# Kernel optimization log

Hardware: AMD Instinct MI355X
Metric: run time of the kernel (lower is better)

Reference implementation:

```python
import jax, jax.numpy as jnp
import numpy as np


def setup_inputs() -> dict:
    key = jax.random.key(0)
    k1, k2, k3 = jax.random.split(key, 3)
    b, n, d, f = 16, 2048, 256, 256
    features = jax.random.normal(k1, (b, n, d), dtype=jnp.float32)
    # dense adjacency; row-normalize like MeanAggregator's normalized A
    A = jax.random.uniform(k2, (b, n, n), dtype=jnp.float32)
    A = A / jnp.sum(A, axis=-1, keepdims=True)
    weight = jax.random.normal(k3, (2 * d, f), dtype=jnp.float32) * (1.0 / np.sqrt(2 * d))
    bias = jnp.zeros((f,), dtype=jnp.float32)
    return {"features": features, "A": A, "weight": weight, "bias": bias}


def reference(features, A, weight, bias):
    # agg = A @ features  (MeanAggregator: row-normalized adjacency)
    agg = jnp.einsum('bnm,bmd->bnd', A, features)  # [b,n,d]
    d = features.shape[-1]
    # split-weight GEMM instead of materializing concat:
    # [feat, agg] @ W == feat @ W[:d] + agg @ W[d:]
    out = (jnp.einsum('bnd,df->bnf', features, weight[:d])
           + jnp.einsum('bnd,df->bnf', agg, weight[d:])
           + bias)
    return jax.nn.relu(out)
```

## Files before the change

### kernel.cpp

```cpp
#include <hip/hip_runtime.h>

typedef __attribute__((ext_vector_type(8))) short bf16x8;
typedef __attribute__((ext_vector_type(4))) float f32x4;

__device__ __forceinline__ unsigned short f2bf(float f) {
    unsigned int u = __builtin_bit_cast(unsigned int, f);
    unsigned int r = (u + 0x7FFFu + ((u >> 16) & 1u)) >> 16;
    return (unsigned short)r;
}

__device__ __forceinline__ void gll16(const void* g, void* l) {
    __builtin_amdgcn_global_load_lds(
        (const __attribute__((address_space(1))) void*)g,
        (__attribute__((address_space(3))) void*)l, 16, 0, 0);
}

__global__ __launch_bounds__(256) void transpose_cvt_kernel(
    const float* __restrict__ src, unsigned short* __restrict__ dstT,
    unsigned short* __restrict__ dstS, int R, int C)
{
    __shared__ float tile[64][65];
    const int b = blockIdx.z;
    const float* s = src + (size_t)b * R * C;
    const int r0 = blockIdx.x * 64, c0 = blockIdx.y * 64;
    const int t = threadIdx.x;
    const int r = t >> 2, cg = (t & 3) * 16;

    float v[16];
    const float4* p = reinterpret_cast<const float4*>(s + (size_t)(r0 + r) * C + c0 + cg);
#pragma unroll
    for (int i = 0; i < 4; ++i) {
        float4 q = p[i];
        v[4 * i + 0] = q.x; v[4 * i + 1] = q.y; v[4 * i + 2] = q.z; v[4 * i + 3] = q.w;
    }
#pragma unroll
    for (int i = 0; i < 16; ++i) tile[r][cg + i] = v[i];

    if (dstS) {
        unsigned int w[8];
#pragma unroll
        for (int i = 0; i < 8; ++i)
            w[i] = (unsigned)f2bf(v[2 * i]) | ((unsigned)f2bf(v[2 * i + 1]) << 16);
        unsigned int* d = reinterpret_cast<unsigned int*>(
            dstS + (size_t)b * R * C + (size_t)(r0 + r) * C + c0 + cg);
        *reinterpret_cast<uint4*>(d)     = make_uint4(w[0], w[1], w[2], w[3]);
        *reinterpret_cast<uint4*>(d + 4) = make_uint4(w[4], w[5], w[6], w[7]);
    }

    __syncthreads();

    const int cl = t >> 2, rg = (t & 3) * 16;
    unsigned int w[8];
#pragma unroll
    for (int i = 0; i < 8; ++i) {
        unsigned short lo = f2bf(tile[rg + 2 * i][cl]);
        unsigned short hi = f2bf(tile[rg + 2 * i + 1][cl]);
        w[i] = (unsigned)lo | ((unsigned)hi << 16);
    }
    unsigned int* d = reinterpret_cast<unsigned int*>(
        dstT + (size_t)b * R * C + (size_t)(c0 + cl) * R + r0 + rg);
    *reinterpret_cast<uint4*>(d)     = make_uint4(w[0], w[1], w[2], w[3]);
    *reinterpret_cast<uint4*>(d + 4) = make_uint4(w[4], w[5], w[6], w[7]);
}

__global__ __launch_bounds__(512, 2) void k1_agg_gemm(
    const float* __restrict__ A, const unsigned short* __restrict__ Ft,
    unsigned short* __restrict__ agg)
{
    __shared__ short Ab[2][128][64];
    __shared__ short Bb[2][256][64];

    const int tid = threadIdx.x;
    const int lane = tid & 63, wid = tid >> 6;
    const int wr = wid >> 2, wc = wid & 3;
    const int lo = lane & 15, hi = lane >> 4;
    const int batch = blockIdx.y, mt = blockIdx.x;

    const float* Abase = A + ((size_t)batch * 2048 + (size_t)mt * 128) * 2048;
    const unsigned short* Fbase = Ft + (size_t)batch * 256 * 2048;

    const int arow = tid >> 2;
    const int acg = tid & 3;

    f32x4 acc[4][4];
#pragma unroll
    for (int m = 0; m < 4; ++m)
#pragma unroll
        for (int n = 0; n < 4; ++n) acc[m][n] = (f32x4){0.f, 0.f, 0.f, 0.f};

    float va[16];

    auto load_A = [&](int k0) {
        const float4* p = reinterpret_cast<const float4*>(
            Abase + (size_t)arow * 2048 + k0 + acg * 16);
#pragma unroll
        for (int i = 0; i < 4; ++i) {
            float4 q = p[i];
            va[4 * i + 0] = q.x; va[4 * i + 1] = q.y; va[4 * i + 2] = q.z; va[4 * i + 3] = q.w;
        }
    };
    auto write_A = [&](int buf) {
#pragma unroll
        for (int j = 0; j < 2; ++j) {
            unsigned int w[4];
#pragma unroll
            for (int i = 0; i < 4; ++i) {
                int e = j * 8 + i * 2;
                w[i] = (unsigned)f2bf(va[e]) | ((unsigned)f2bf(va[e + 1]) << 16);
            }
            int slin = acg * 2 + j;
            int off = arow * 64 + ((slin ^ (arow & 7)) << 3);
            *reinterpret_cast<uint4*>(&Ab[buf][0][0] + off) = make_uint4(w[0], w[1], w[2], w[3]);
        }
    };
    auto stage_B = [&](int buf, int k0) {
#pragma unroll
        for (int it = 0; it < 4; ++it) {
            int si = it * 512 + tid;
            int row = si >> 3, slot = si & 7;
            const unsigned short* g = Fbase + (size_t)row * 2048 + k0 + ((slot ^ (row & 7)) << 3);
            short* l = &Bb[buf][0][0] + (size_t)(it * 512 + (wid << 6)) * 8;
            gll16(g, l);
        }
    };

    load_A(0);
    stage_B(0, 0);
    write_A(0);
    __syncthreads();

    for (int t = 0; t < 32; ++t) {
        const int cur = t & 1;
        const int nxt = cur ^ 1;
        const bool has_next = (t + 1) < 32;
        if (has_next) {
            load_A((t + 1) * 64);
            stage_B(nxt, (t + 1) * 64);
        }
#pragma unroll
        for (int kk = 0; kk < 2; ++kk) {
            bf16x8 af[4], bfv[4];
#pragma unroll
            for (int m = 0; m < 4; ++m) {
                int row = wr * 64 + m * 16 + lo;
                int off = row * 64 + (((kk * 4 + hi) ^ (row & 7)) << 3);
                af[m] = *reinterpret_cast<const bf16x8*>(&Ab[cur][0][0] + off);
            }
#pragma unroll
            for (int n = 0; n < 4; ++n) {
                int row = wc * 64 + n * 16 + lo;
                int off = row * 64 + (((kk * 4 + hi) ^ (row & 7)) << 3);
                bfv[n] = *reinterpret_cast<const bf16x8*>(&Bb[cur][0][0] + off);
            }
#pragma unroll
            for (int m = 0; m < 4; ++m)
#pragma unroll
                for (int n = 0; n < 4; ++n)
                    acc[m][n] = __builtin_amdgcn_mfma_f32_16x16x32_bf16(af[m], bfv[n], acc[m][n], 0, 0, 0);
        }
        if (has_next) write_A(nxt);
        __syncthreads();
    }

    unsigned short* obase = agg + ((size_t)batch * 2048 + (size_t)mt * 128) * 256;
#pragma unroll
    for (int m = 0; m < 4; ++m) {
#pragma unroll
        for (int n = 0; n < 4; ++n) {
            int col = wc * 64 + n * 16 + lo;
#pragma unroll
            for (int j = 0; j < 4; ++j) {
                int row = wr * 64 + m * 16 + hi * 4 + j;
                obase[(size_t)row * 256 + col] = f2bf(acc[m][n][j]);
            }
        }
    }
}

__global__ __launch_bounds__(512, 2) void k2_out_gemm(
    const unsigned short* __restrict__ Fb, const unsigned short* __restrict__ aggp,
    const unsigned short* __restrict__ Wt, const float* __restrict__ bias,
    float* __restrict__ out)
{
    __shared__ short Ab[2][128][64];
    __shared__ short Bb[2][256][64];

    const int tid = threadIdx.x;
    const int lane = tid & 63, wid = tid >> 6;
    const int wr = wid >> 2, wc = wid & 3;
    const int lo = lane & 15, hi = lane >> 4;
    const int m0 = blockIdx.x * 128;

    auto stage_A = [&](int buf, int k0) {
        const unsigned short* src = (k0 < 256) ? Fb : aggp;
        const int kk0 = k0 & 255;
#pragma unroll
        for (int it = 0; it < 2; ++it) {
            int si = it * 512 + tid;
            int row = si >> 3, slot = si & 7;
            const unsigned short* g = src + (size_t)(m0 + row) * 256 + kk0 + ((slot ^ (row & 7)) << 3);
            short* l = &Ab[buf][0][0] + (size_t)(it * 512 + (wid << 6)) * 8;
            gll16(g, l);
        }
    };
    auto stage_B = [&](int buf, int k0) {
#pragma unroll
        for (int it = 0; it < 4; ++it) {
            int si = it * 512 + tid;
            int row = si >> 3, slot = si & 7;
            const unsigned short* g = Wt + (size_t)row * 512 + k0 + ((slot ^ (row & 7)) << 3);
            short* l = &Bb[buf][0][0] + (size_t)(it * 512 + (wid << 6)) * 8;
            gll16(g, l);
        }
    };

    f32x4 acc[4][4];
#pragma unroll
    for (int m = 0; m < 4; ++m)
#pragma unroll
        for (int n = 0; n < 4; ++n) acc[m][n] = (f32x4){0.f, 0.f, 0.f, 0.f};

    stage_A(0, 0);
    stage_B(0, 0);
    __syncthreads();

    for (int t = 0; t < 8; ++t) {
        const int cur = t & 1;
        const int nxt = cur ^ 1;
        const bool has_next = (t + 1) < 8;
        if (has_next) {
            stage_A(nxt, (t + 1) * 64);
            stage_B(nxt, (t + 1) * 64);
        }
#pragma unroll
        for (int kk = 0; kk < 2; ++kk) {
            bf16x8 af[4], bfv[4];
#pragma unroll
            for (int m = 0; m < 4; ++m) {
                int row = wr * 64 + m * 16 + lo;
                int off = row * 64 + (((kk * 4 + hi) ^ (row & 7)) << 3);
                af[m] = *reinterpret_cast<const bf16x8*>(&Ab[cur][0][0] + off);
            }
#pragma unroll
            for (int n = 0; n < 4; ++n) {
                int row = wc * 64 + n * 16 + lo;
                int off = row * 64 + (((kk * 4 + hi) ^ (row & 7)) << 3);
                bfv[n] = *reinterpret_cast<const bf16x8*>(&Bb[cur][0][0] + off);
            }
#pragma unroll
            for (int m = 0; m < 4; ++m)
#pragma unroll
                for (int n = 0; n < 4; ++n)
                    acc[m][n] = __builtin_amdgcn_mfma_f32_16x16x32_bf16(af[m], bfv[n], acc[m][n], 0, 0, 0);
        }
        __syncthreads();
    }

    float bv[4];
#pragma unroll
    for (int n = 0; n < 4; ++n) bv[n] = bias[wc * 64 + n * 16 + lo];

#pragma unroll
    for (int m = 0; m < 4; ++m) {
#pragma unroll
        for (int n = 0; n < 4; ++n) {
            int col = wc * 64 + n * 16 + lo;
#pragma unroll
            for (int j = 0; j < 4; ++j) {
                int row = m0 + wr * 64 + m * 16 + hi * 4 + j;
                float v = acc[m][n][j] + bv[n];
                out[(size_t)row * 256 + col] = fmaxf(v, 0.f);
            }
        }
    }
}

extern "C" void kernel_launch(void* const* d_in, const int* in_sizes, int n_in,
                              void* d_out, int out_size, void* d_ws, size_t ws_size,
                              hipStream_t stream) {
    const float* features = (const float*)d_in[0];
    const float* A        = (const float*)d_in[1];
    const float* weight   = (const float*)d_in[2];
    const float* bias     = (const float*)d_in[3];
    float* out = (float*)d_out;

    const size_t F_ELEMS = (size_t)16 * 2048 * 256;
    const size_t FT_B  = F_ELEMS * 2;
    const size_t FB_B  = F_ELEMS * 2;
    const size_t WT_B  = (size_t)256 * 512 * 2;
    const size_t AGG_B = F_ELEMS * 2;
    if (ws_size < FT_B + FB_B + WT_B + AGG_B) return;

    char* ws = (char*)d_ws;
    unsigned short* Ft  = (unsigned short*)ws;
    unsigned short* Fb  = (unsigned short*)(ws + FT_B);
    unsigned short* Wt  = (unsigned short*)(ws + FT_B + FB_B);
    unsigned short* agg = (unsigned short*)(ws + FT_B + FB_B + WT_B);

    dim3 gF(2048 / 64, 256 / 64, 16);
    transpose_cvt_kernel<<<gF, 256, 0, stream>>>(features, Ft, Fb, 2048, 256);
    dim3 gW(512 / 64, 256 / 64, 1);
    transpose_cvt_kernel<<<gW, 256, 0, stream>>>(weight, Wt, nullptr, 512, 256);

    dim3 g1(16, 16);
    k1_agg_gemm<<<g1, 512, 0, stream>>>(A, Ft, agg);

    k2_out_gemm<<<256, 512, 0, stream>>>(Fb, agg, Wt, bias, out);
}
```

Before: 126.4 us.

## Split-K the aggregation GEMM, single-buffer LDS, and fold partial sums into output GEMM

The aggregation GEMM now splits K in two, launching 512 blocks with an XCD-aware block remap. Each half writes its own bf16 partial buffer, and the output GEMM sums them by running extra K iterations that reuse the bottom half of the weight. Both kernels drop LDS double buffering in favour of single buffers with more resident blocks: k1 gets occupancy 4, and k2 uses 64-row tiles with 256 threads. A cheaper round-half-up bf16 pack replaces round-to-nearest-even for A. Risks are the loss of load/compute overlap, extra global traffic for the second partial buffer, and slightly different rounding.

After: 126.4 us. Within noise of the previous version (-0.0%).

```diff
diff --git a/kernel.cpp b/kernel.cpp
--- a/kernel.cpp
+++ b/kernel.cpp
@@ -7,6 +7,11 @@
     unsigned int u = __builtin_bit_cast(unsigned int, f);
     unsigned int r = (u + 0x7FFFu + ((u >> 16) & 1u)) >> 16;
     return (unsigned short)r;
+}
+__device__ __forceinline__ unsigned int pkbf(float lo, float hi) {
+    unsigned int ul = __builtin_bit_cast(unsigned int, lo) + 0x8000u;
+    unsigned int uh = __builtin_bit_cast(unsigned int, hi) + 0x8000u;
+    return (uh & 0xFFFF0000u) | (ul >> 16);
 }
 
 __device__ __forceinline__ void gll16(const void* g, void* l) {
@@ -63,24 +68,29 @@
     *reinterpret_cast<uint4*>(d + 4) = make_uint4(w[4], w[5], w[6], w[7]);
 }
 
-__global__ __launch_bounds__(512, 2) void k1_agg_gemm(
+__global__ __launch_bounds__(512, 4) void k1_agg_gemm(
     const float* __restrict__ A, const unsigned short* __restrict__ Ft,
-    unsigned short* __restrict__ agg)
+    unsigned short* __restrict__ agg0, unsigned short* __restrict__ agg1)
 {
-    __shared__ short Ab[2][128][64];
-    __shared__ short Bb[2][256][64];
+    __shared__ short Ab[128][64];
+    __shared__ short Bb[256][64];
 
     const int tid = threadIdx.x;
     const int lane = tid & 63, wid = tid >> 6;
     const int wr = wid >> 2, wc = wid & 3;
     const int lo = lane & 15, hi = lane >> 4;
-    const int batch = blockIdx.y, mt = blockIdx.x;
-
-    const float* Abase = A + ((size_t)batch * 2048 + (size_t)mt * 128) * 2048;
-    const unsigned short* Fbase = Ft + (size_t)batch * 256 * 2048;
+
+    const int bid = blockIdx.x;
+    const int wg = ((bid & 7) << 6) | (bid >> 3);
+    const int batch = wg >> 5;
+    const int ks    = (wg >> 4) & 1;
+    const int mt    = wg & 15;
+
+    const float* Abase = A + ((size_t)batch * 2048 + (size_t)mt * 128) * 2048 + (size_t)ks * 1024;
+    const unsigned short* Fbase = Ft + (size_t)batch * 256 * 2048 + (size_t)ks * 1024;
 
     const int arow = tid >> 2;
-    const int acg = tid & 3;
+    const int acg  = tid & 3;
 
     f32x4 acc[4][4];
 #pragma unroll
@@ -88,55 +98,32 @@
 #pragma unroll
         for (int n = 0; n < 4; ++n) acc[m][n] = (f32x4){0.f, 0.f, 0.f, 0.f};
 
-    float va[16];
-
-    auto load_A = [&](int k0) {
+    for (int t = 0; t < 16; ++t) {
+        const int k0 = t * 64;
         const float4* p = reinterpret_cast<const float4*>(
             Abase + (size_t)arow * 2048 + k0 + acg * 16);
-#pragma unroll
-        for (int i = 0; i < 4; ++i) {
-            float4 q = p[i];
-            va[4 * i + 0] = q.x; va[4 * i + 1] = q.y; va[4 * i + 2] = q.z; va[4 * i + 3] = q.w;
-        }
-    };
-    auto write_A = [&](int buf) {
-#pragma unroll
-        for (int j = 0; j < 2; ++j) {
-            unsigned int w[4];
-#pragma unroll
-            for (int i = 0; i < 4; ++i) {
-                int e = j * 8 + i * 2;
-                w[i] = (unsigned)f2bf(va[e]) | ((unsigned)f2bf(va[e + 1]) << 16);
-            }
-            int slin = acg * 2 + j;
-            int off = arow * 64 + ((slin ^ (arow & 7)) << 3);
-            *reinterpret_cast<uint4*>(&Ab[buf][0][0] + off) = make_uint4(w[0], w[1], w[2], w[3]);
-        }
-    };
-    auto stage_B = [&](int buf, int k0) {
+        float4 q0 = p[0], q1 = p[1], q2 = p[2], q3 = p[3];
 #pragma unroll
         for (int it = 0; it < 4; ++it) {
             int si = it * 512 + tid;
             int row = si >> 3, slot = si & 7;
             const unsigned short* g = Fbase + (size_t)row * 2048 + k0 + ((slot ^ (row & 7)) << 3);
-            short* l = &Bb[buf][0][0] + (size_t)(it * 512 + (wid << 6)) * 8;
+            short* l = &Bb[0][0] + (size_t)(it * 512 + (wid << 6)) * 8;
             gll16(g, l);
         }
-    };
-
-    load_A(0);
-    stage_B(0, 0);
-    write_A(0);
-    __syncthreads();
-
-    for (int t = 0; t < 32; ++t) {
-        const int cur = t & 1;
-        const int nxt = cur ^ 1;
-        const bool has_next = (t + 1) < 32;
-        if (has_next) {
-            load_A((t + 1) * 64);
-            stage_B(nxt, (t + 1) * 64);
-        }
+        unsigned int w0 = pkbf(q0.x, q0.y), w1 = pkbf(q0.z, q0.w);
+        unsigned int w2 = pkbf(q1.x, q1.y), w3 = pkbf(q1.z, q1.w);
+        unsigned int w4 = pkbf(q2.x, q2.y), w5 = pkbf(q2.z, q2.w);
+        unsigned int w6 = pkbf(q3.x, q3.y), w7 = pkbf(q3.z, q3.w);
+        {
+            int slin = acg * 2;
+            int off0 = arow * 64 + (((slin    ) ^ (arow & 7)) << 3);
+            int off1 = arow * 64 + (((slin + 1) ^ (arow & 7)) << 3);
+            *reinterpret_cast<uint4*>(&Ab[0][0] + off0) = make_uint4(w0, w1, w2, w3);
+            *reinterpret_cast<uint4*>(&Ab[0][0] + off1) = make_uint4(w4, w5, w6, w7);
+        }
+        __syncthreads();
+
 #pragma unroll
         for (int kk = 0; kk < 2; ++kk) {
             bf16x8 af[4], bfv[4];
@@ -144,13 +131,13 @@
             for (int m = 0; m < 4; ++m) {
                 int row = wr * 64 + m * 16 + lo;
                 int off = row * 64 + (((kk * 4 + hi) ^ (row & 7)) << 3);
-                af[m] = *reinterpret_cast<const bf16x8*>(&Ab[cur][0][0] + off);
+                af[m] = *reinterpret_cast<const bf16x8*>(&Ab[0][0] + off);
             }
 #pragma unroll
             for (int n = 0; n < 4; ++n) {
                 int row = wc * 64 + n * 16 + lo;
                 int off = row * 64 + (((kk * 4 + hi) ^ (row & 7)) << 3);
-                bfv[n] = *reinterpret_cast<const bf16x8*>(&Bb[cur][0][0] + off);
+                bfv[n] = *reinterpret_cast<const bf16x8*>(&Bb[0][0] + off);
             }
 #pragma unroll
             for (int m = 0; m < 4; ++m)
@@ -158,11 +145,11 @@
                 for (int n = 0; n < 4; ++n)
                     acc[m][n] = __builtin_amdgcn_mfma_f32_16x16x32_bf16(af[m], bfv[n], acc[m][n], 0, 0, 0);
         }
-        if (has_next) write_A(nxt);
-        __syncthreads();
-    }
-
-    unsigned short* obase = agg + ((size_t)batch * 2048 + (size_t)mt * 128) * 256;
+        __syncthreads();
+    }
+
+    unsigned short* obase = (ks ? agg1 : agg0)
+        + ((size_t)batch * 2048 + (size_t)mt * 128) * 256;
 #pragma unroll
     for (int m = 0; m < 4; ++m) {
 #pragma unroll
@@ -177,75 +164,63 @@
     }
 }
 
-__global__ __launch_bounds__(512, 2) void k2_out_gemm(
-    const unsigned short* __restrict__ Fb, const unsigned short* __restrict__ aggp,
-    const unsigned short* __restrict__ Wt, const float* __restrict__ bias,
-    float* __restrict__ out)
+__global__ __launch_bounds__(256, 2) void k2_out_gemm(
+    const unsigned short* __restrict__ Fb, const unsigned short* __restrict__ agg0,
+    const unsigned short* __restrict__ agg1, const unsigned short* __restrict__ Wt,
+    const float* __restrict__ bias, float* __restrict__ out)
 {
-    __shared__ short Ab[2][128][64];
-    __shared__ short Bb[2][256][64];
+    __shared__ short Ab[64][64];
+    __shared__ short Bb[256][64];
 
     const int tid = threadIdx.x;
     const int lane = tid & 63, wid = tid >> 6;
-    const int wr = wid >> 2, wc = wid & 3;
+    const int wc = wid;
     const int lo = lane & 15, hi = lane >> 4;
-    const int m0 = blockIdx.x * 128;
-
-    auto stage_A = [&](int buf, int k0) {
-        const unsigned short* src = (k0 < 256) ? Fb : aggp;
-        const int kk0 = k0 & 255;
+    const int m0 = blockIdx.x * 64;
+
+    f32x4 acc[4][4];
+#pragma unroll
+    for (int m = 0; m < 4; ++m)
+#pragma unroll
+        for (int n = 0; n < 4; ++n) acc[m][n] = (f32x4){0.f, 0.f, 0.f, 0.f};
+
+    for (int t = 0; t < 12; ++t) {
+        const int k0 = t * 64;
+        const unsigned short* asrc = (k0 < 256) ? Fb : (k0 < 512 ? agg0 : agg1);
+        const int ak = k0 & 255;
 #pragma unroll
         for (int it = 0; it < 2; ++it) {
-            int si = it * 512 + tid;
+            int si = it * 256 + tid;
             int row = si >> 3, slot = si & 7;
-            const unsigned short* g = src + (size_t)(m0 + row) * 256 + kk0 + ((slot ^ (row & 7)) << 3);
-            short* l = &Ab[buf][0][0] + (size_t)(it * 512 + (wid << 6)) * 8;
+            const unsigned short* g = asrc + (size_t)(m0 + row) * 256 + ak + ((slot ^ (row & 7)) << 3);
+            short* l = &Ab[0][0] + (size_t)(it * 256 + (wid << 6)) * 8;
             gll16(g, l);
         }
-    };
-    auto stage_B = [&](int buf, int k0) {
-#pragma unroll
-        for (int it = 0; it < 4; ++it) {
-            int si = it * 512 + tid;
+        const int bk = (k0 < 512) ? k0 : k0 - 256;
+#pragma unroll
+        for (int it = 0; it < 8; ++it) {
+            int si = it * 256 + tid;
             int row = si >> 3, slot = si & 7;
-            const unsigned short* g = Wt + (size_t)row * 512 + k0 + ((slot ^ (row & 7)) << 3);
-            short* l = &Bb[buf][0][0] + (size_t)(it * 512 + (wid << 6)) * 8;
+            const unsigned short* g = Wt + (size_t)row * 512 + bk + ((slot ^ (row & 7)) << 3);
+            short* l = &Bb[0][0] + (size_t)(it * 256 + (wid << 6)) * 8;
             gll16(g, l);
         }
-    };
-
-    f32x4 acc[4][4];
-#pragma unroll
-    for (int m = 0; m < 4; ++m)
-#pragma unroll
-        for (int n = 0; n < 4; ++n) acc[m][n] = (f32x4){0.f, 0.f, 0.f, 0.f};
-
-    stage_A(0, 0);
-    stage_B(0, 0);
-    __syncthreads();
-
-    for (int t = 0; t < 8; ++t) {
-        const int cur = t & 1;
-        const int nxt = cur ^ 1;
-        const bool has_next = (t + 1) < 8;
-        if (has_next) {
-            stage_A(nxt, (t + 1) * 64);
-            stage_B(nxt, (t + 1) * 64);
-        }
+        __syncthreads();
+
 #pragma unroll
         for (int kk = 0; kk < 2; ++kk) {
             bf16x8 af[4], bfv[4];
 #pragma unroll
             for (int m = 0; m < 4; ++m) {
-                int row = wr * 64 + m * 16 + lo;
-                int off = row * 64 + (((kk * 4 + hi) ^ (row & 7)) << 3);
-                af[m] = *reinterpret_cast<const bf16x8*>(&Ab[cur][0][0] + off);
+                int row = m * 16 + lo;
+                int off = row * 64 + (((kk * 4 + hi) ^ (row & 7)) << 3);
+                af[m] = *reinterpret_cast<const bf16x8*>(&Ab[0][0] + off);
             }
 #pragma unroll
             for (int n = 0; n < 4; ++n) {
                 int row = wc * 64 + n * 16 + lo;
                 int off = row * 64 + (((kk * 4 + hi) ^ (row & 7)) << 3);
-                bfv[n] = *reinterpret_cast<const bf16x8*>(&Bb[cur][0][0] + off);
+                bfv[n] = *reinterpret_cast<const bf16x8*>(&Bb[0][0] + off);
             }
 #pragma unroll
             for (int m = 0; m < 4; ++m)
@@ -267,7 +242,7 @@
             int col = wc * 64 + n * 16 + lo;
 #pragma unroll
             for (int j = 0; j < 4; ++j) {
-                int row = m0 + wr * 64 + m * 16 + hi * 4 + j;
+                int row = m0 + m * 16 + hi * 4 + j;
                 float v = acc[m][n][j] + bv[n];
                 out[(size_t)row * 256 + col] = fmaxf(v, 0.f);
             }
@@ -285,25 +260,25 @@
     float* out = (float*)d_out;
 
     const size_t F_ELEMS = (size_t)16 * 2048 * 256;
-    const size_t FT_B  = F_ELEMS * 2;
-    const size_t FB_B  = F_ELEMS * 2;
-    const size_t WT_B  = (size_t)256 * 512 * 2;
-    const size_t AGG_B = F_ELEMS * 2;
-    if (ws_size < FT_B + FB_B + WT_B + AGG_B) return;
+    const size_t FT_B   = F_ELEMS * 2;
+    const size_t FB_B   = F_ELEMS * 2;
+    const size_t WT_B   = (size_t)256 * 512 * 2;
+    const size_t AGG_B  = F_ELEMS * 2;
+    if (ws_size < FT_B + FB_B + WT_B + 2 * AGG_B) return;
 
     char* ws = (char*)d_ws;
-    unsigned short* Ft  = (unsigned short*)ws;
-    unsigned short* Fb  = (unsigned short*)(ws + FT_B);
-    unsigned short* Wt  = (unsigned short*)(ws + FT_B + FB_B);
-    unsigned short* agg = (unsigned short*)(ws + FT_B + FB_B + WT_B);
+    unsigned short* Ft   = (unsigned short*)ws;
+    unsigned short* Fb   = (unsigned short*)(ws + FT_B);
+    unsigned short* Wt   = (unsigned short*)(ws + FT_B + FB_B);
+    unsigned short* agg0 = (unsigned short*)(ws + FT_B + FB_B + WT_B);
+    unsigned short* agg1 = (unsigned short*)(ws + FT_B + FB_B + WT_B + AGG_B);
 
     dim3 gF(2048 / 64, 256 / 64, 16);
     transpose_cvt_kernel<<<gF, 256, 0, stream>>>(features, Ft, Fb, 2048, 256);
     dim3 gW(512 / 64, 256 / 64, 1);
     transpose_cvt_kernel<<<gW, 256, 0, stream>>>(weight, Wt, nullptr, 512, 256);
 
-    dim3 g1(16, 16);
-    k1_agg_gemm<<<g1, 512, 0, stream>>>(A, Ft, agg);
-
-    k2_out_gemm<<<256, 512, 0, stream>>>(Fb, agg, Wt, bias, out);
-}
+    k1_agg_gemm<<<512, 512, 0, stream>>>(A, Ft, agg0, agg1);
+
+    k2_out_gemm<<<512, 256, 0, stream>>>(Fb, agg0, agg1, Wt, bias, out);
+}
```
